# Kernel tuning notes

Hardware: AMD Instinct MI355X
Metric: run time of the kernel (lower is better)

The kernel has to match this reference:

```python
import jax, jax.numpy as jnp
import numpy as np

NP_CONST = 48.0  # Np in the original code


def dft_matrices(freq=48, time=512):
    # A[t, f] = exp(-2j*pi*t*f/time)/sqrt(time), split into re/im, shape [time, freq]
    t = np.arange(time)[:, None]
    f = np.arange(freq)[None, :]
    ang = -2.0 * np.pi * t * f / time
    scale = 1.0 / np.sqrt(time)
    return (np.cos(ang) * scale).astype(np.float32), (np.sin(ang) * scale).astype(np.float32)


def _mm(xr, xi, wr, wi):
    # complex matmul: (xr + i xi) @ (wr + i wi)
    return xr @ wr - xi @ wi, xr @ wi + xi @ wr


def _act(R, sigma, theta):
    # scaled soft-threshold (standard LAMP shrinkage); returns f and df/dR
    lam = theta[0] * sigma
    mag = jnp.abs(R)
    shr = jnp.maximum(mag - lam, 0.0)
    f = theta[1] * jnp.sign(R) * shr
    df = theta[1] * (mag > lam).astype(R.dtype)
    return f, df


def setup_inputs() -> dict:
    key = jax.random.key(0)
    L, B = 8, 8192
    dre, dim = dft_matrices(48, 512)
    u = jax.random.normal(key, (B, 48, 2), dtype=jnp.float32)
    # per-layer params initialized to the DFT matrices (as in LAMP_layer.__init__)
    A_re = jnp.broadcast_to(jnp.asarray(dre), (L, 512, 48)).copy()
    A_im = jnp.broadcast_to(jnp.asarray(dim), (L, 512, 48)).copy()
    theta = jnp.broadcast_to(jnp.array([1.0, 1.0, -1.0], dtype=jnp.float32), (L, 3)).copy()
    return {"u": u, "A_re": A_re, "A_im": A_im, "theta": theta,
            "DFT_re": jnp.asarray(dre), "DFT_im": jnp.asarray(dim)}


def _lamp_forward(u, A_re, A_im, theta, DFT_re, DFT_im):
    u_re, u_im = u[:, :, 0], u[:, :, 1]          # [B, 48]
    B = u_re.shape[0]
    z_re, z_im = u_re, u_im
    H_re = jnp.zeros((B, 512), dtype=u.dtype)
    H_im = jnp.zeros((B, 512), dtype=u.dtype)

    def layer(carry, params):
        z_re, z_im, H_re, H_im = carry
        Are, Aim, th = params                      # [512,48], [512,48], [3]
        # Z = z @ A.T : [B,48] x [48,512]
        Z_re, Z_im = _mm(z_re, z_im, Are.T, Aim.T)
        R_re = H_re + Z_re
        R_im = H_im + Z_im
        sigma = jnp.sqrt(jnp.sum(z_re * z_re) + jnp.sum(z_im * z_im)) / jnp.sqrt(NP_CONST)
        Hn_re, d_re = _act(R_re, sigma, th)
        Hn_im, d_im = _act(R_im, sigma, th)
        b_re = d_re.sum() / NP_CONST
        b_im = d_im.sum() / NP_CONST
        # h_hat = H_hat @ A : [B,512] x [512,48]
        h_re, h_im = _mm(Hn_re, Hn_im, Are, Aim)
        zn_re = u_re - h_re + b_re * z_re
        zn_im = u_im - h_im + b_im * z_im
        return (zn_re, zn_im, Hn_re, Hn_im), None

    (z_re, z_im, H_re, H_im), _ = jax.lax.scan(layer, (z_re, z_im, H_re, H_im),
                                               (A_re, A_im, theta))
    h_re, h_im = _mm(H_re, H_im, DFT_re, DFT_im)   # [B, 48]
    return jnp.stack((h_re, h_im), axis=2)          # [B, 48, 2]


def reference(u, A_re, A_im, theta, DFT_re, DFT_im):
    return _lamp_forward(u, A_re, A_im, theta, DFT_re, DFT_im)
```

## Files before the change

kernel.cpp:

```cpp
#include <hip/hip_runtime.h>
#include <hip/hip_bf16.h>
#include <math.h>

#define B_   8192
#define F_   48
#define T_   512
#define L_   8
#define NBLK 256
#define THR  512
#define NW   8
#define RPB  32
#define HST  520
#define ZS   52
#define LINE 32
#define NEVT 8
#define VALS_OFF LINE
#define SYNC_DW  (LINE + NEVT * 8 * LINE)

typedef unsigned short ushort_t;
typedef unsigned int   uint_t;
typedef __attribute__((ext_vector_type(8))) short short8;
typedef __attribute__((ext_vector_type(4))) float f32x4;

#define MFMA(a,b,c) __builtin_amdgcn_mfma_f32_16x16x32_bf16(a,b,c,0,0,0)

__device__ inline ushort_t f2bf(float x) {
    __hip_bfloat16 h = __float2bfloat16(x);
    return *reinterpret_cast<ushort_t*>(&h);
}
__device__ inline short8 negbf(short8 v) {
    short8 r;
    #pragma unroll
    for (int i = 0; i < 8; ++i) r[i] = v[i] ^ (short)0x8000;
    return r;
}
__device__ inline short8 pack8(float4 a, float4 b) {
    short8 r;
    r[0]=(short)f2bf(a.x); r[1]=(short)f2bf(a.y); r[2]=(short)f2bf(a.z); r[3]=(short)f2bf(a.w);
    r[4]=(short)f2bf(b.x); r[5]=(short)f2bf(b.y); r[6]=(short)f2bf(b.z); r[7]=(short)f2bf(b.w);
    return r;
}

__device__ inline float aload(const float* p) {
    return __hip_atomic_load(p, __ATOMIC_RELAXED, __HIP_MEMORY_SCOPE_AGENT);
}
__device__ inline void afadd(float* p, float v) {
    (void)__hip_atomic_fetch_add(p, v, __ATOMIC_RELAXED, __HIP_MEMORY_SCOPE_AGENT);
}
__device__ inline void bar_add(uint_t* cnt) {
    (void)__hip_atomic_fetch_add(cnt, 1u, __ATOMIC_RELEASE, __HIP_MEMORY_SCOPE_AGENT);
}
__device__ inline void bar_wait(uint_t* cnt, uint_t tgt) {
    if (threadIdx.x == 0) {
        while (__hip_atomic_load(cnt, __ATOMIC_RELAXED, __HIP_MEMORY_SCOPE_AGENT) < tgt)
            __builtin_amdgcn_s_sleep(2);
        (void)__hip_atomic_load(cnt, __ATOMIC_ACQUIRE, __HIP_MEMORY_SCOPE_AGENT);
    }
    __syncthreads();
}

__global__ __launch_bounds__(256) void k_pre(
    const float* __restrict__ Ar, const float* __restrict__ Ai,
    const float* __restrict__ Dr, const float* __restrict__ Di,
    ushort_t* __restrict__ Afr, ushort_t* __restrict__ Afi,
    ushort_t* __restrict__ Atr, ushort_t* __restrict__ Ati,
    ushort_t* __restrict__ Dfr, ushort_t* __restrict__ Dfi,
    uint_t* __restrict__ syncbuf)
{
    const int gt = blockIdx.x * 256 + threadIdx.x;
    const int gs = gridDim.x * 256;
    if (gt < SYNC_DW) syncbuf[gt] = 0u;
    for (int idx = gt; idx < L_ * 32768; idx += gs) {
        int j = idx & 7, rest = idx >> 3;
        int mm = rest & 15; rest >>= 4;
        int qq = rest & 3;  rest >>= 2;
        int k2 = rest & 1;  rest >>= 1;
        int tile = rest & 31;
        int l = rest >> 5;
        int t = tile * 16 + mm, k = k2 * 32 + qq * 8 + j;
        float vr = 0.f, vi = 0.f;
        if (k < 48) { int g = l * 24576 + t * 48 + k; vr = Ar[g]; vi = Ai[g]; }
        Afr[idx] = f2bf(vr); Afi[idx] = f2bf(vi);
    }
    for (int idx = gt; idx < L_ * 24576; idx += gs) {
        int j = idx & 7, rest = idx >> 3;
        int mm = rest & 15; rest >>= 4;
        int qq = rest & 3;  rest >>= 2;
        int ks = rest & 15; rest >>= 4;
        int ft = rest % 3;
        int l = rest / 3;
        int f = ft * 16 + mm, k = ks * 32 + qq * 8 + j;
        int g = l * 24576 + k * 48 + f;
        Atr[idx] = f2bf(Ar[g]); Ati[idx] = f2bf(Ai[g]);
    }
    for (int idx = gt; idx < 24576; idx += gs) {
        int j = idx & 7, rest = idx >> 3;
        int mm = rest & 15; rest >>= 4;
        int qq = rest & 3;  rest >>= 2;
        int ks = rest & 15;
        int ft = rest >> 4;
        int f = ft * 16 + mm, k = ks * 32 + qq * 8 + j;
        Dfr[idx] = f2bf(Dr[k * 48 + f]); Dfi[idx] = f2bf(Di[k * 48 + f]);
    }
}

__global__ __launch_bounds__(THR, 2) void k_lamp(
    const float* __restrict__ u,
    const ushort_t* __restrict__ Afr, const ushort_t* __restrict__ Afi,
    const ushort_t* __restrict__ Atr, const ushort_t* __restrict__ Ati,
    const ushort_t* __restrict__ Dfr, const ushort_t* __restrict__ Dfi,
    const float* __restrict__ th,
    uint_t* syncbuf,
    float* __restrict__ out)
{
    extern __shared__ char dyn[];
    float*    pR   = (float*)dyn;
    float*    pI   = pR + 8 * 3 * 16 * 17;
    float*    zreL = pI + 8 * 3 * 16 * 17;
    float*    zimL = zreL + RPB * ZS;
    float*    red  = zimL + RPB * ZS;
    ushort_t* HreL = (ushort_t*)(red + 128);
    ushort_t* HimL = HreL + RPB * HST;

    uint_t* cnt  = syncbuf;
    float*  vals = (float*)syncbuf + VALS_OFF;
    auto vslot = [&](int e, int j) { return vals + (size_t)(e * 8 + j) * LINE; };

    const int tid = threadIdx.x, blk = blockIdx.x;
    const int row0 = blk * RPB;
    const int wave = tid >> 6, lane = tid & 63;
    const int quad = lane >> 4, m = lane & 15;
    const int rows16 = (wave >> 2) * 16;
    const int rt = wave >> 2, kq = wave & 3;
    const float2* u2 = (const float2*)u;
    uint_t tgt = 0;

    f32x4 hR[8], hI[8];
    #pragma unroll
    for (int ct = 0; ct < 8; ++ct) { hR[ct] = (f32x4){0,0,0,0}; hI[ct] = (f32x4){0,0,0,0}; }

    float uRe[3], uIm[3];
    float acc = 0.f;
    #pragma unroll
    for (int k3 = 0; k3 < 3; ++k3) {
        int j = tid + k3 * THR;
        int r = j / 48, c = j - r * 48;
        float2 v = u2[(row0 + r) * 48 + c];
        uRe[k3] = v.x; uIm[k3] = v.y;
        zreL[r * ZS + c] = v.x; zimL[r * ZS + c] = v.y;
        acc += v.x * v.x + v.y * v.y;
    }
    #pragma unroll
    for (int o = 32; o > 0; o >>= 1) acc += __shfl_xor(acc, o, 64);
    __syncthreads();
    if (lane == 0) red[16 + wave] = acc;
    __syncthreads();
    if (tid == 0) {
        float t = 0.f;
        #pragma unroll
        for (int w = 0; w < NW; ++w) t += red[16 + w];
        afadd(vslot(0, 0), t); bar_add(cnt);
    }
    tgt += NBLK;

    float lam = 0.f;
    for (int l = 0; l < L_; ++l) {
        const float th1 = th[l * 3 + 1];

        const float* zpr = zreL + (rows16 + m) * ZS;
        const float* zpi = zimL + (rows16 + m) * ZS;
        short8 zr0 = pack8(*(const float4*)(zpr + quad * 8), *(const float4*)(zpr + quad * 8 + 4));
        short8 zi0 = pack8(*(const float4*)(zpi + quad * 8), *(const float4*)(zpi + quad * 8 + 4));
        short8 zr1 = {0,0,0,0,0,0,0,0}, zi1 = {0,0,0,0,0,0,0,0};
        if (quad < 2) {
            zr1 = pack8(*(const float4*)(zpr + 32 + quad * 8), *(const float4*)(zpr + 36 + quad * 8));
            zi1 = pack8(*(const float4*)(zpi + 32 + quad * 8), *(const float4*)(zpi + 36 + quad * 8));
        }
        short8 zin0 = negbf(zi0), zin1 = negbf(zi1);

        const ushort_t* Aflr = Afr + (size_t)l * 32768;
        const ushort_t* Afli = Afi + (size_t)l * 32768;
        #pragma unroll
        for (int ct = 0; ct < 8; ++ct) {
            const int tile = (wave & 3) * 8 + ct;
            const ushort_t* rp = Aflr + (size_t)(tile * 2) * 512 + lane * 8;
            const ushort_t* ip = Afli + (size_t)(tile * 2) * 512 + lane * 8;
            short8 ar0 = *(const short8*)rp;
            short8 ar1 = *(const short8*)(rp + 512);
            short8 ai0 = *(const short8*)ip;
            short8 ai1 = *(const short8*)(ip + 512);
            hR[ct] = MFMA(zr0, ar0, hR[ct]);
            hR[ct] = MFMA(zr1, ar1, hR[ct]);
            hR[ct] = MFMA(zin0, ai0, hR[ct]);
            hR[ct] = MFMA(zin1, ai1, hR[ct]);
            hI[ct] = MFMA(zr0, ai0, hI[ct]);
            hI[ct] = MFMA(zr1, ai1, hI[ct]);
            hI[ct] = MFMA(zi0, ar0, hI[ct]);
            hI[ct] = MFMA(zi1, ar1, hI[ct]);
        }

        if (l == 0) {
            bar_wait(cnt, tgt);
            lam = th[0] * sqrtf(aload(vslot(0, 0)) * (1.0f / 48.0f));
        }

        float cr = 0.f, ci = 0.f;
        #pragma unroll
        for (int ct = 0; ct < 8; ++ct) {
            const int t = ((wave & 3) * 8 + ct) * 16 + m;
            #pragma unroll
            for (int reg = 0; reg < 4; ++reg) {
                const int lr = rows16 + quad * 4 + reg;
                float Rr = hR[ct][reg], Ri = hI[ct][reg];
                float mr = fabsf(Rr), mi = fabsf(Ri);
                float fr = th1 * copysignf(fmaxf(mr - lam, 0.f), Rr);
                float fi = th1 * copysignf(fmaxf(mi - lam, 0.f), Ri);
                cr += (mr > lam) ? 1.f : 0.f;
                ci += (mi > lam) ? 1.f : 0.f;
                hR[ct][reg] = fr; hI[ct][reg] = fi;
                HreL[lr * HST + t] = f2bf(fr);
                HimL[lr * HST + t] = f2bf(fi);
            }
        }

        if (l == L_ - 1) { __syncthreads(); break; }
        __syncthreads();

        const ushort_t* Atlr = Atr + (size_t)l * 24576;
        const ushort_t* Atli = Ati + (size_t)l * 24576;
        f32x4 aR[3], aI[3];
        #pragma unroll
        for (int q = 0; q < 3; ++q) { aR[q] = (f32x4){0,0,0,0}; aI[q] = (f32x4){0,0,0,0}; }
        #pragma unroll
        for (int ks = 0; ks < 4; ++ks) {
            const int ksa = kq * 4 + ks;
            const int k0 = ksa * 32 + quad * 8;
            short8 hr = *(const short8*)&HreL[(rt * 16 + m) * HST + k0];
            short8 hi = *(const short8*)&HimL[(rt * 16 + m) * HST + k0];
            short8 hin = negbf(hi);
            #pragma unroll
            for (int ft = 0; ft < 3; ++ft) {
                short8 br = *(const short8*)(Atlr + (size_t)((ft * 16 + ksa) * 64 + lane) * 8);
                short8 bi = *(const short8*)(Atli + (size_t)((ft * 16 + ksa) * 64 + lane) * 8);
                aR[ft] = MFMA(hr, br, aR[ft]);
                aR[ft] = MFMA(hin, bi, aR[ft]);
                aI[ft] = MFMA(hr, bi, aI[ft]);
                aI[ft] = MFMA(hi, br, aI[ft]);
            }
        }
        #pragma unroll
        for (int ft = 0; ft < 3; ++ft) {
            #pragma unroll
            for (int reg = 0; reg < 4; ++reg) {
                pR[((wave * 3 + ft) * 16 + quad * 4 + reg) * 17 + m] = aR[ft][reg];
                pI[((wave * 3 + ft) * 16 + quad * 4 + reg) * 17 + m] = aI[ft][reg];
            }
        }
        __syncthreads();

        float aRe[3], aIm[3], zR3[3], zI3[3];
        float S1 = 0.f, S2 = 0.f, S3 = 0.f, S4 = 0.f, S5 = 0.f, S6 = 0.f;
        #pragma unroll
        for (int k3 = 0; k3 < 3; ++k3) {
            int j = tid + k3 * THR;
            int r = j / 48, f = j - r * 48;
            int rt2 = r >> 4, lr = r & 15, ft = f >> 4, c = f & 15;
            float hRv = 0.f, hIv = 0.f;
            #pragma unroll
            for (int q = 0; q < 4; ++q) {
                hRv += pR[(((rt2 * 4 + q) * 3 + ft) * 16 + lr) * 17 + c];
                hIv += pI[(((rt2 * 4 + q) * 3 + ft) * 16 + lr) * 17 + c];
            }
            float zr = zreL[r * ZS + f], zi = zimL[r * ZS + f];
            float ar = uRe[k3] - hRv, ai = uIm[k3] - hIv;
            aRe[k3] = ar; aIm[k3] = ai; zR3[k3] = zr; zI3[k3] = zi;
            S1 += ar * ar; S2 += ar * zr; S3 += zr * zr;
            S4 += ai * ai; S5 += ai * zi; S6 += zi * zi;
        }

        float v8[8] = {cr, ci, S1, S2, S3, S4, S5, S6};
        #pragma unroll
        for (int j = 0; j < 8; ++j) {
            #pragma unroll
            for (int o = 32; o > 0; o >>= 1) v8[j] += __shfl_xor(v8[j], o, 64);
        }
        if (lane == 0) {
            #pragma unroll
            for (int j = 0; j < 8; ++j) red[16 + wave * 8 + j] = v8[j];
        }
        __syncthreads();
        if (tid == 0) {
            #pragma unroll
            for (int j = 0; j < 8; ++j) {
                float s = 0.f;
                #pragma unroll
                for (int w = 0; w < NW; ++w) s += red[16 + w * 8 + j];
                afadd(vslot(l + 1, j), s);
            }
            bar_add(cnt);
        }
        tgt += NBLK;
        bar_wait(cnt, tgt);

        const float CR = aload(vslot(l + 1, 0));
        const float CI = aload(vslot(l + 1, 1));
        const float G1 = aload(vslot(l + 1, 2));
        const float G2 = aload(vslot(l + 1, 3));
        const float G3 = aload(vslot(l + 1, 4));
        const float G4 = aload(vslot(l + 1, 5));
        const float G5 = aload(vslot(l + 1, 6));
        const float G6 = aload(vslot(l + 1, 7));
        const float bre = th1 * CR * (1.0f / 48.0f);
        const float bim = th1 * CI * (1.0f / 48.0f);
        const float sig2 = G1 + 2.f * bre * G2 + bre * bre * G3
                         + G4 + 2.f * bim * G5 + bim * bim * G6;
        lam = th[(l + 1) * 3] * sqrtf(sig2 * (1.0f / 48.0f));

        #pragma unroll
        for (int k3 = 0; k3 < 3; ++k3) {
            int j = tid + k3 * THR;
            int r = j / 48, f = j - r * 48;
            zreL[r * ZS + f] = aRe[k3] + bre * zR3[k3];
            zimL[r * ZS + f] = aIm[k3] + bim * zI3[k3];
        }
        __syncthreads();
    }

    f32x4 fR[3], fI[3];
    #pragma unroll
    for (int q = 0; q < 3; ++q) { fR[q] = (f32x4){0,0,0,0}; fI[q] = (f32x4){0,0,0,0}; }
    #pragma unroll
    for (int ks = 0; ks < 4; ++ks) {
        const int ksa = kq * 4 + ks;
        const int k0 = ksa * 32 + quad * 8;
        short8 hr = *(const short8*)&HreL[(rt * 16 + m) * HST + k0];
        short8 hi = *(const short8*)&HimL[(rt * 16 + m) * HST + k0];
        short8 hin = negbf(hi);
        #pragma unroll
        for (int ft = 0; ft < 3; ++ft) {
            short8 br = *(const short8*)(Dfr + (size_t)((ft * 16 + ksa) * 64 + lane) * 8);
            short8 bi = *(const short8*)(Dfi + (size_t)((ft * 16 + ksa) * 64 + lane) * 8);
            fR[ft] = MFMA(hr, br, fR[ft]);
            fR[ft] = MFMA(hin, bi, fR[ft]);
            fI[ft] = MFMA(hr, bi, fI[ft]);
            fI[ft] = MFMA(hi, br, fI[ft]);
        }
    }
    #pragma unroll
    for (int ft = 0; ft < 3; ++ft) {
        #pragma unroll
        for (int reg = 0; reg < 4; ++reg) {
            pR[((wave * 3 + ft) * 16 + quad * 4 + reg) * 17 + m] = fR[ft][reg];
            pI[((wave * 3 + ft) * 16 + quad * 4 + reg) * 17 + m] = fI[ft][reg];
        }
    }
    __syncthreads();
    float2* out2 = (float2*)out;
    #pragma unroll
    for (int k3 = 0; k3 < 3; ++k3) {
        int j = tid + k3 * THR;
        int r = j / 48, f = j - r * 48;
        int rt2 = r >> 4, lr = r & 15, ft = f >> 4, c = f & 15;
        float hRv = 0.f, hIv = 0.f;
        #pragma unroll
        for (int q = 0; q < 4; ++q) {
            hRv += pR[(((rt2 * 4 + q) * 3 + ft) * 16 + lr) * 17 + c];
            hIv += pI[(((rt2 * 4 + q) * 3 + ft) * 16 + lr) * 17 + c];
        }
        out2[(row0 + r) * 48 + f] = make_float2(hRv, hIv);
    }
}

extern "C" void kernel_launch(void* const* d_in, const int* in_sizes, int n_in,
                              void* d_out, int out_size, void* d_ws, size_t ws_size,
                              hipStream_t stream) {
    (void)in_sizes; (void)n_in; (void)out_size; (void)ws_size;
    const float* u  = (const float*)d_in[0];
    const float* Ar = (const float*)d_in[1];
    const float* Ai = (const float*)d_in[2];
    const float* th = (const float*)d_in[3];
    const float* Dr = (const float*)d_in[4];
    const float* Di = (const float*)d_in[5];
    float* out = (float*)d_out;

    char* p = (char*)d_ws;
    auto alloc = [&](size_t bytes) -> char* {
        char* r = p;
        p += (bytes + 255) & ~(size_t)255;
        return r;
    };
    uint_t*   syncbuf = (uint_t*)alloc((size_t)SYNC_DW * 4);
    ushort_t* Afr = (ushort_t*)alloc((size_t)L_ * 32768 * 2);
    ushort_t* Afi = (ushort_t*)alloc((size_t)L_ * 32768 * 2);
    ushort_t* Atr = (ushort_t*)alloc((size_t)L_ * 24576 * 2);
    ushort_t* Ati = (ushort_t*)alloc((size_t)L_ * 24576 * 2);
    ushort_t* Dfr = (ushort_t*)alloc((size_t)24576 * 2);
    ushort_t* Dfi = (ushort_t*)alloc((size_t)24576 * 2);

    k_pre<<<1024, 256, 0, stream>>>(Ar, Ai, Dr, Di, Afr, Afi, Atr, Ati, Dfr, Dfi, syncbuf);

    const uint_t lds_bytes = 132608;
    hipFuncSetAttribute((const void*)k_lamp,
                        hipFuncAttributeMaxDynamicSharedMemorySize, (int)lds_bytes);
    void* args[] = { (void*)&u, (void*)&Afr, (void*)&Afi, (void*)&Atr, (void*)&Ati,
                     (void*)&Dfr, (void*)&Dfi, (void*)&th,
                     (void*)&syncbuf, (void*)&out };
    hipLaunchCooperativeKernel((void*)k_lamp, dim3(NBLK), dim3(THR), args,
                               lds_bytes, stream);
}
```

Before: 291.4 us.

## Overlap grid barrier with next layer matmul via linear split of z update

```diff
diff --git a/kernel.cpp b/kernel.cpp
--- a/kernel.cpp
+++ b/kernel.cpp
@@ -118,7 +118,9 @@
     float*    pI   = pR + 8 * 3 * 16 * 17;
     float*    zreL = pI + 8 * 3 * 16 * 17;
     float*    zimL = zreL + RPB * ZS;
-    float*    red  = zimL + RPB * ZS;
+    float*    aReL = zimL + RPB * ZS;
+    float*    aImL = aReL + RPB * ZS;
+    float*    red  = aImL + RPB * ZS;
     ushort_t* HreL = (ushort_t*)(red + 128);
     ushort_t* HimL = HreL + RPB * HST;
 
@@ -133,20 +135,17 @@
     const int rows16 = (wave >> 2) * 16;
     const int rt = wave >> 2, kq = wave & 3;
     const float2* u2 = (const float2*)u;
-    uint_t tgt = 0;
 
     f32x4 hR[8], hI[8];
     #pragma unroll
     for (int ct = 0; ct < 8; ++ct) { hR[ct] = (f32x4){0,0,0,0}; hI[ct] = (f32x4){0,0,0,0}; }
 
-    float uRe[3], uIm[3];
     float acc = 0.f;
     #pragma unroll
     for (int k3 = 0; k3 < 3; ++k3) {
         int j = tid + k3 * THR;
         int r = j / 48, c = j - r * 48;
         float2 v = u2[(row0 + r) * 48 + c];
-        uRe[k3] = v.x; uIm[k3] = v.y;
         zreL[r * ZS + c] = v.x; zimL[r * ZS + c] = v.y;
         acc += v.x * v.x + v.y * v.y;
     }
@@ -161,11 +160,12 @@
         for (int w = 0; w < NW; ++w) t += red[16 + w];
         afadd(vslot(0, 0), t); bar_add(cnt);
     }
-    tgt += NBLK;
 
     float lam = 0.f;
     for (int l = 0; l < L_; ++l) {
         const float th1 = th[l * 3 + 1];
+        const ushort_t* Aflr = Afr + (size_t)l * 32768;
+        const ushort_t* Afli = Afi + (size_t)l * 32768;
 
         const float* zpr = zreL + (rows16 + m) * ZS;
         const float* zpi = zimL + (rows16 + m) * ZS;
@@ -176,32 +176,116 @@
             zr1 = pack8(*(const float4*)(zpr + 32 + quad * 8), *(const float4*)(zpr + 36 + quad * 8));
             zi1 = pack8(*(const float4*)(zpi + 32 + quad * 8), *(const float4*)(zpi + 36 + quad * 8));
         }
-        short8 zin0 = negbf(zi0), zin1 = negbf(zi1);
-
-        const ushort_t* Aflr = Afr + (size_t)l * 32768;
-        const ushort_t* Afli = Afi + (size_t)l * 32768;
-        #pragma unroll
-        for (int ct = 0; ct < 8; ++ct) {
-            const int tile = (wave & 3) * 8 + ct;
-            const ushort_t* rp = Aflr + (size_t)(tile * 2) * 512 + lane * 8;
-            const ushort_t* ip = Afli + (size_t)(tile * 2) * 512 + lane * 8;
-            short8 ar0 = *(const short8*)rp;
-            short8 ar1 = *(const short8*)(rp + 512);
-            short8 ai0 = *(const short8*)ip;
-            short8 ai1 = *(const short8*)(ip + 512);
-            hR[ct] = MFMA(zr0, ar0, hR[ct]);
-            hR[ct] = MFMA(zr1, ar1, hR[ct]);
-            hR[ct] = MFMA(zin0, ai0, hR[ct]);
-            hR[ct] = MFMA(zin1, ai1, hR[ct]);
-            hI[ct] = MFMA(zr0, ai0, hI[ct]);
-            hI[ct] = MFMA(zr1, ai1, hI[ct]);
-            hI[ct] = MFMA(zi0, ar0, hI[ct]);
-            hI[ct] = MFMA(zi1, ar1, hI[ct]);
-        }
 
         if (l == 0) {
-            bar_wait(cnt, tgt);
+            short8 zin0 = negbf(zi0), zin1 = negbf(zi1);
+            #pragma unroll
+            for (int ct = 0; ct < 8; ++ct) {
+                const int tile = (wave & 3) * 8 + ct;
+                const ushort_t* rp = Aflr + (size_t)(tile * 2) * 512 + lane * 8;
+                const ushort_t* ip = Afli + (size_t)(tile * 2) * 512 + lane * 8;
+                short8 ar0 = *(const short8*)rp;
+                short8 ar1 = *(const short8*)(rp + 512);
+                short8 ai0 = *(const short8*)ip;
+                short8 ai1 = *(const short8*)(ip + 512);
+                hR[ct] = MFMA(zr0, ar0, hR[ct]);
+                hR[ct] = MFMA(zr1, ar1, hR[ct]);
+                hR[ct] = MFMA(zin0, ai0, hR[ct]);
+                hR[ct] = MFMA(zin1, ai1, hR[ct]);
+                hI[ct] = MFMA(zr0, ai0, hI[ct]);
+                hI[ct] = MFMA(zr1, ai1, hI[ct]);
+                hI[ct] = MFMA(zi0, ar0, hI[ct]);
+                hI[ct] = MFMA(zi1, ar1, hI[ct]);
+            }
+            bar_wait(cnt, (uint_t)NBLK);
             lam = th[0] * sqrtf(aload(vslot(0, 0)) * (1.0f / 48.0f));
+        } else {
+            f32x4 Q1[8], Q2[8], Q3[8], Q4[8];
+            #pragma unroll
+            for (int ct = 0; ct < 8; ++ct) {
+                Q1[ct] = (f32x4){0,0,0,0}; Q2[ct] = (f32x4){0,0,0,0};
+                Q3[ct] = (f32x4){0,0,0,0}; Q4[ct] = (f32x4){0,0,0,0};
+            }
+            #pragma unroll
+            for (int ct = 0; ct < 8; ++ct) {
+                const int tile = (wave & 3) * 8 + ct;
+                const ushort_t* rp = Aflr + (size_t)(tile * 2) * 512 + lane * 8;
+                const ushort_t* ip = Afli + (size_t)(tile * 2) * 512 + lane * 8;
+                short8 ar0 = *(const short8*)rp;
+                short8 ar1 = *(const short8*)(rp + 512);
+                short8 ai0 = *(const short8*)ip;
+                short8 ai1 = *(const short8*)(ip + 512);
+                Q1[ct] = MFMA(zr0, ar0, Q1[ct]);
+                Q1[ct] = MFMA(zr1, ar1, Q1[ct]);
+                Q2[ct] = MFMA(zi0, ai0, Q2[ct]);
+                Q2[ct] = MFMA(zi1, ai1, Q2[ct]);
+                Q3[ct] = MFMA(zr0, ai0, Q3[ct]);
+                Q3[ct] = MFMA(zr1, ai1, Q3[ct]);
+                Q4[ct] = MFMA(zi0, ar0, Q4[ct]);
+                Q4[ct] = MFMA(zi1, ar1, Q4[ct]);
+            }
+
+            const float* apr = aReL + (rows16 + m) * ZS;
+            const float* api = aImL + (rows16 + m) * ZS;
+            short8 aa0 = pack8(*(const float4*)(apr + quad * 8), *(const float4*)(apr + quad * 8 + 4));
+            short8 ab0 = pack8(*(const float4*)(api + quad * 8), *(const float4*)(api + quad * 8 + 4));
+            short8 aa1 = {0,0,0,0,0,0,0,0}, ab1 = {0,0,0,0,0,0,0,0};
+            if (quad < 2) {
+                aa1 = pack8(*(const float4*)(apr + 32 + quad * 8), *(const float4*)(apr + 36 + quad * 8));
+                ab1 = pack8(*(const float4*)(api + 32 + quad * 8), *(const float4*)(api + 36 + quad * 8));
+            }
+            short8 abn0 = negbf(ab0), abn1 = negbf(ab1);
+            #pragma unroll
+            for (int ct = 0; ct < 8; ++ct) {
+                const int tile = (wave & 3) * 8 + ct;
+                const ushort_t* rp = Aflr + (size_t)(tile * 2) * 512 + lane * 8;
+                const ushort_t* ip = Afli + (size_t)(tile * 2) * 512 + lane * 8;
+                short8 ar0 = *(const short8*)rp;
+                short8 ar1 = *(const short8*)(rp + 512);
+                short8 ai0 = *(const short8*)ip;
+                short8 ai1 = *(const short8*)(ip + 512);
+                hR[ct] = MFMA(aa0, ar0, hR[ct]);
+                hR[ct] = MFMA(aa1, ar1, hR[ct]);
+                hR[ct] = MFMA(abn0, ai0, hR[ct]);
+                hR[ct] = MFMA(abn1, ai1, hR[ct]);
+                hI[ct] = MFMA(aa0, ai0, hI[ct]);
+                hI[ct] = MFMA(aa1, ai1, hI[ct]);
+                hI[ct] = MFMA(ab0, ar0, hI[ct]);
+                hI[ct] = MFMA(ab1, ar1, hI[ct]);
+            }
+
+            bar_wait(cnt, (uint_t)NBLK * (uint_t)(l + 1));
+            const float thp = th[(l - 1) * 3 + 1];
+            const float CR = aload(vslot(l, 0));
+            const float CI = aload(vslot(l, 1));
+            const float G1 = aload(vslot(l, 2));
+            const float G2 = aload(vslot(l, 3));
+            const float G3 = aload(vslot(l, 4));
+            const float G4 = aload(vslot(l, 5));
+            const float G5 = aload(vslot(l, 6));
+            const float G6 = aload(vslot(l, 7));
+            const float bre = thp * CR * (1.0f / 48.0f);
+            const float bim = thp * CI * (1.0f / 48.0f);
+            const float sig2 = G1 + 2.f * bre * G2 + bre * bre * G3
+                             + G4 + 2.f * bim * G5 + bim * bim * G6;
+            lam = th[l * 3] * sqrtf(sig2 * (1.0f / 48.0f));
+
+            #pragma unroll
+            for (int ct = 0; ct < 8; ++ct) {
+                #pragma unroll
+                for (int r = 0; r < 4; ++r) {
+                    hR[ct][r] += bre * Q1[ct][r] - bim * Q2[ct][r];
+                    hI[ct][r] += bre * Q3[ct][r] + bim * Q4[ct][r];
+                }
+            }
+
+            #pragma unroll
+            for (int k3 = 0; k3 < 3; ++k3) {
+                int j = tid + k3 * THR;
+                int r = j / 48, f = j - r * 48;
+                zreL[r * ZS + f] = aReL[r * ZS + f] + bre * zreL[r * ZS + f];
+                zimL[r * ZS + f] = aImL[r * ZS + f] + bim * zimL[r * ZS + f];
+            }
         }
 
         float cr = 0.f, ci = 0.f;
@@ -258,7 +342,6 @@
         }
         __syncthreads();
 
-        float aRe[3], aIm[3], zR3[3], zI3[3];
         float S1 = 0.f, S2 = 0.f, S3 = 0.f, S4 = 0.f, S5 = 0.f, S6 = 0.f;
         #pragma unroll
         for (int k3 = 0; k3 < 3; ++k3) {
@@ -271,9 +354,10 @@
                 hRv += pR[(((rt2 * 4 + q) * 3 + ft) * 16 + lr) * 17 + c];
                 hIv += pI[(((rt2 * 4 + q) * 3 + ft) * 16 + lr) * 17 + c];
             }
+            float2 uv = u2[(row0 + r) * 48 + f];
             float zr = zreL[r * ZS + f], zi = zimL[r * ZS + f];
-            float ar = uRe[k3] - hRv, ai = uIm[k3] - hIv;
-            aRe[k3] = ar; aIm[k3] = ai; zR3[k3] = zr; zI3[k3] = zi;
+            float ar = uv.x - hRv, ai = uv.y - hIv;
+            aReL[r * ZS + f] = ar; aImL[r * ZS + f] = ai;
             S1 += ar * ar; S2 += ar * zr; S3 += zr * zr;
             S4 += ai * ai; S5 += ai * zi; S6 += zi * zi;
         }
@@ -299,31 +383,6 @@
             }
             bar_add(cnt);
         }
-        tgt += NBLK;
-        bar_wait(cnt, tgt);
-
-        const float CR = aload(vslot(l + 1, 0));
-        const float CI = aload(vslot(l + 1, 1));
-        const float G1 = aload(vslot(l + 1, 2));
-        const float G2 = aload(vslot(l + 1, 3));
-        const float G3 = aload(vslot(l + 1, 4));
-        const float G4 = aload(vslot(l + 1, 5));
-        const float G5 = aload(vslot(l + 1, 6));
-        const float G6 = aload(vslot(l + 1, 7));
-        const float bre = th1 * CR * (1.0f / 48.0f);
-        const float bim = th1 * CI * (1.0f / 48.0f);
-        const float sig2 = G1 + 2.f * bre * G2 + bre * bre * G3
-                         + G4 + 2.f * bim * G5 + bim * bim * G6;
-        lam = th[(l + 1) * 3] * sqrtf(sig2 * (1.0f / 48.0f));
-
-        #pragma unroll
-        for (int k3 = 0; k3 < 3; ++k3) {
-            int j = tid + k3 * THR;
-            int r = j / 48, f = j - r * 48;
-            zreL[r * ZS + f] = aRe[k3] + bre * zR3[k3];
-            zimL[r * ZS + f] = aIm[k3] + bim * zI3[k3];
-        }
-        __syncthreads();
     }
 
     f32x4 fR[3], fI[3];
@@ -399,7 +458,7 @@
 
     k_pre<<<1024, 256, 0, stream>>>(Ar, Ai, Dr, Di, Afr, Afi, Atr, Ati, Dfr, Dfi, syncbuf);
 
-    const uint_t lds_bytes = 132608;
+    const uint_t lds_bytes = 145920;
     hipFuncSetAttribute((const void*)k_lamp,
                         hipFuncAttributeMaxDynamicSharedMemorySize, (int)lds_bytes);
     void* args[] = { (void*)&u, (void*)&Afr, (void*)&Afi, (void*)&Atr, (void*)&Ati,
```

Result: slower. 586.1 us (+101.1%).
